# Kernel optimization log

Hardware: AMD Instinct MI355X
Metric: run time of the kernel (lower is better)

The kernel has to match this reference:

```python
import jax, jax.numpy as jnp
import numpy as np

WIDTH, DEPTH = 2048, 8
TIME_MOD = 30 * DEPTH + 2  # 242


def setup_inputs() -> dict:
    key = jax.random.key(0)
    ks = jax.random.split(key, 7)
    s = float(np.sqrt(1.0 / WIDTH))
    so = float(np.sqrt(1.0 / (WIDTH + DEPTH + 1)))
    return {
        "x": jax.random.normal(ks[0], (WIDTH,), dtype=jnp.float32),
        "weights": jax.random.uniform(ks[1], (WIDTH, WIDTH, DEPTH), minval=-s, maxval=s, dtype=jnp.float32),
        "output_weights": jax.random.uniform(ks[2], (WIDTH, DEPTH + 1), minval=-so, maxval=so, dtype=jnp.float32),
        "state": jax.random.uniform(ks[3], (WIDTH, DEPTH + 1), dtype=jnp.float32),  # relu outputs >= 0
        "stored_activations": jax.random.uniform(ks[4], (WIDTH, DEPTH + 1, TIME_MOD), dtype=jnp.float32),
        "stored_gradiets": jax.random.normal(ks[5], (WIDTH, DEPTH), dtype=jnp.float32),
        "output_gradient": jax.random.normal(ks[6], (WIDTH, DEPTH + 1, TIME_MOD), dtype=jnp.float32),
        "time": 7,
    }


def reference(x, weights, output_weights, state, stored_activations, stored_gradiets, output_gradient, time):
    width, dp1 = state.shape
    depth = dp1 - 1
    mod = 30 * depth + 2
    dt = state.dtype

    # recurrent state update: state[w,d] = relu(sum_i weights[i,w,d] * state_prev[i,d])
    hidden = jax.nn.relu(jnp.einsum("iwd,id->wd", weights, state[:, :depth]))
    state = jnp.concatenate([x[:, None], hidden], axis=1)  # (W, depth+1)
    output = jnp.sum(output_weights * state)

    # scatter into circular buffers at slot `time` (static int)
    sa = stored_activations.at[:, :, time].set(state)
    og = output_gradient.at[:, :, time].set(output_weights)

    # stored gradients: loop over a reads only OLD stored_gradiets[:, a+1] -> vectorizable
    a = np.arange(depth - 1)  # a = 0 .. depth-2 (static indices)
    t_idx = (time - 2 * depth + 2 * (a + 1)) % mod  # (depth-1,)
    relu_m = (sa[:, a + 2, (t_idx + 1) % mod] > 0).astype(dt)  # (W, depth-1)
    contrib = jnp.einsum("ija,ja->ia", weights[:, :, 1:depth], stored_gradiets[:, 1:depth])
    sg_head = relu_m * contrib + og[:, a + 1, t_idx]  # (W, depth-1)
    sg_last = og[:, depth, time]  # a == depth-1 branch (time_index == time)
    sg = jnp.concatenate([sg_head, sg_last[:, None]], axis=1)  # (W, depth)

    output_weights_gradient = state

    # weight eligibility traces (uses UPDATED sa and UPDATED sg)
    aa = np.arange(depth)
    tia = (time - 2 * depth + 2 * (aa + 1)) % mod  # (depth,)
    relu_g = (sa[:, aa + 1, tia] > 0).astype(dt)  # (W, depth)
    act_prev = sa[:, aa, (tia - 1) % mod]  # (W, depth)
    gradients = act_prev[:, None, :] * (sg * relu_g)[None, :, :]  # (W, W, depth)

    return output, state, sa, sg, og, gradients, output_weights_gradient
```

## Files before the change

### kernel.cpp

```cpp
#include <hip/hip_runtime.h>

#define MOD 242

static constexpr long long OFF_STATE = 1;
static constexpr long long OFF_SA    = 18433;
static constexpr long long OFF_SG    = 4478977;
static constexpr long long OFF_OG    = 4495361;
static constexpr long long OFF_GRAD  = 8955905;
static constexpr long long OFF_OWG   = 42510337;

#define WS_HID  0
#define WS_CON  524288
#define WS_COL  786432
#define WS_ROW  802816
#define WS_OUTP 819200

template <int CTRL, int RM>
__device__ __forceinline__ float dppadd(float x) {
  int t = __builtin_amdgcn_update_dpp(0, __float_as_int(x), CTRL, RM, 0xF, true);
  return x + __int_as_float(t);
}
__device__ __forceinline__ float wave_sum_dpp(float x) {
  x = dppadd<0x111, 0xF>(x);
  x = dppadd<0x112, 0xF>(x);
  x = dppadd<0x114, 0xF>(x);
  x = dppadd<0x118, 0xF>(x);
  x = dppadd<0x142, 0xA>(x);
  x = dppadd<0x143, 0xC>(x);
  return x;
}

__global__ __launch_bounds__(256) void k_mvcopy(
    const float* __restrict__ weights, const float* __restrict__ state,
    const float* __restrict__ sgrad, const float* __restrict__ sa_in,
    const float* __restrict__ og_in, float* __restrict__ ws,
    float* __restrict__ out)
{
  const int b   = blockIdx.x;
  const int tid = threadIdx.x;

  if (b >= 512) {
    const unsigned g = (unsigned)(b - 512) * 256u + (unsigned)tid;
    for (size_t e = g; e < 4460544u; e += 1114112u) {
      out[OFF_SA + e] = sa_in[e];
      out[OFF_OG + e] = og_in[e];
    }
    return;
  }

  const int iblk = b & 31;
  const int wblk = b >> 5;
  const int i0   = iblk * 64;
  const int w0   = wblk * 128;
  const int wv   = tid >> 6;
  const int l    = tid & 63;
  const int wgrp = wv >> 1;
  const int dh   = wv & 1;
  const int w    = w0 + wgrp * 64 + l;

  __shared__ __align__(16) float state_lds[64 * 8];
  __shared__ __align__(16) float cl[4][64][4];

  for (int idx = tid; idx < 64 * 8; idx += 256)
    state_lds[idx] = state[(size_t)(i0 + (idx >> 3)) * 9 + (idx & 7)];
  __syncthreads();

  const float4 sg4 = *(const float4*)&sgrad[(size_t)w * 8 + dh * 4];
  float4 h4 = make_float4(0.f, 0.f, 0.f, 0.f);
  const float* wp = weights + ((size_t)i0 * 2048 + w) * 8 + dh * 4;

  #pragma unroll 4
  for (int ii = 0; ii < 64; ++ii) {
    const float4 w4 = *(const float4*)wp;
    wp += 16384;
    const float4 s4 = *(const float4*)&state_lds[ii * 8 + dh * 4];

    h4.x = fmaf(w4.x, s4.x, h4.x);
    h4.y = fmaf(w4.y, s4.y, h4.y);
    h4.z = fmaf(w4.z, s4.z, h4.z);
    h4.w = fmaf(w4.w, s4.w, h4.w);

    float vx = wave_sum_dpp(w4.x * sg4.x);
    float vy = wave_sum_dpp(w4.y * sg4.y);
    float vz = wave_sum_dpp(w4.z * sg4.z);
    float vw = wave_sum_dpp(w4.w * sg4.w);
    if (l == 63)
      *(float4*)&cl[wv][ii][0] = make_float4(vx, vy, vz, vw);
  }

  *(float4*)&ws[WS_HID + ((size_t)iblk * 2048 + w) * 8 + dh * 4] = h4;

  __syncthreads();
  {
    const int ii = tid >> 2, q = tid & 3;
    const float c0 = cl[0][ii][q] + cl[2][ii][q];
    const float c1 = cl[1][ii][q] + cl[3][ii][q];
    const size_t base = WS_CON + ((size_t)wblk * 2048 + i0 + ii) * 8;
    ws[base + q]     = c0;
    ws[base + 4 + q] = c1;
  }
}

__global__ __launch_bounds__(64) void k_finalize(
    const float* __restrict__ x, const float* __restrict__ ow,
    const float* __restrict__ sa_in, const float* __restrict__ og_in,
    const int* __restrict__ timep, float* __restrict__ ws, float* __restrict__ out)
{
  const int r = blockIdx.x * 64 + threadIdx.x;
  const int t = *timep;

  float hid[8] = {0,0,0,0,0,0,0,0};
  {
    const float4* hp = (const float4*)&ws[WS_HID + (size_t)r * 8];
    #pragma unroll
    for (int ib = 0; ib < 32; ++ib) {
      const float4 pa = hp[(size_t)ib * 4096];
      const float4 pb = hp[(size_t)ib * 4096 + 1];
      hid[0] += pa.x; hid[1] += pa.y; hid[2] += pa.z; hid[3] += pa.w;
      hid[4] += pb.x; hid[5] += pb.y; hid[6] += pb.z; hid[7] += pb.w;
    }
  }
  float con[8] = {0,0,0,0,0,0,0,0};
  {
    const float4* cp = (const float4*)&ws[WS_CON + (size_t)r * 8];
    #pragma unroll
    for (int wb = 0; wb < 16; ++wb) {
      const float4 pa = cp[(size_t)wb * 4096];
      const float4 pb = cp[(size_t)wb * 4096 + 1];
      con[0] += pa.x; con[1] += pa.y; con[2] += pa.z; con[3] += pa.w;
      con[4] += pb.x; con[5] += pb.y; con[6] += pb.z; con[7] += pb.w;
    }
  }

  float s[9];
  s[0] = x[r];
  #pragma unroll
  for (int d = 0; d < 8; ++d) s[d + 1] = fmaxf(hid[d], 0.f);

  float owr[9];
  #pragma unroll
  for (int c = 0; c < 9; ++c) owr[c] = ow[(size_t)r * 9 + c];

  float p = 0.f;
  #pragma unroll
  for (int c = 0; c < 9; ++c) {
    out[OFF_STATE + (size_t)r * 9 + c] = s[c];
    out[OFF_OWG   + (size_t)r * 9 + c] = s[c];
    out[OFF_SA + ((size_t)r * 9 + c) * MOD + t] = s[c];
    out[OFF_OG + ((size_t)r * 9 + c) * MOD + t] = owr[c];
    p = fmaf(owr[c], s[c], p);
  }
  #pragma unroll
  for (int m = 1; m < 64; m <<= 1) p += __shfl_xor(p, m);
  if (threadIdx.x == 0) ws[WS_OUTP + blockIdx.x] = p;

  float sg[8];
  #pragma unroll
  for (int a = 0; a < 7; ++a) {
    const int ti = (t + 2 * a - 14 + MOD) % MOD;
    const int tm = (ti + 1) % MOD;
    const float av  = (tm == t) ? s[a + 2] : sa_in[((size_t)r * 9 + a + 2) * MOD + tm];
    const float ogv = (ti == t) ? owr[a + 1] : og_in[((size_t)r * 9 + a + 1) * MOD + ti];
    sg[a] = (av > 0.f ? con[a + 1] : 0.f) + ogv;
  }
  sg[7] = owr[8];
  #pragma unroll
  for (int a = 0; a < 8; ++a) out[OFF_SG + (size_t)r * 8 + a] = sg[a];

  #pragma unroll
  for (int aa = 0; aa < 8; ++aa) {
    const int ti = (t + 2 * aa - 14 + MOD) % MOD;
    const int tp = (ti - 1 + MOD) % MOD;
    const float rv = (ti == t) ? s[aa + 1] : sa_in[((size_t)r * 9 + aa + 1) * MOD + ti];
    const float ap = (tp == t) ? s[aa]     : sa_in[((size_t)r * 9 + aa) * MOD + tp];
    ws[WS_COL + r * 8 + aa] = (rv > 0.f) ? sg[aa] : 0.f;
    ws[WS_ROW + r * 8 + aa] = ap;
  }
}

__global__ __launch_bounds__(256) void k_grad(
    const float* __restrict__ ws, float* __restrict__ out)
{
  const int i = blockIdx.x;
  const int tid = threadIdx.x;
  if (i == 0 && tid == 0) {
    float s = 0.f;
    #pragma unroll
    for (int k = 0; k < 32; ++k) s += ws[WS_OUTP + k];
    out[0] = s;
  }
  const float rf = ws[WS_ROW + i * 8 + (tid & 7)];
  float* o = out + OFF_GRAD + (size_t)i * 16384;
  const float* cf = ws + WS_COL;
  #pragma unroll 4
  for (int k = 0; k < 64; ++k) {
    const int e = k * 256 + tid;
    o[e] = rf * cf[e];
  }
}

extern "C" void kernel_launch(void* const* d_in, const int* in_sizes, int n_in,
                              void* d_out, int out_size, void* d_ws, size_t ws_size,
                              hipStream_t stream)
{
  (void)in_sizes; (void)n_in; (void)out_size; (void)ws_size;
  const float* x     = (const float*)d_in[0];
  const float* wts   = (const float*)d_in[1];
  const float* ow    = (const float*)d_in[2];
  const float* st    = (const float*)d_in[3];
  const float* sa_in = (const float*)d_in[4];
  const float* sgrad = (const float*)d_in[5];
  const float* og_in = (const float*)d_in[6];
  const int*   timep = (const int*)d_in[7];
  float* out = (float*)d_out;
  float* ws  = (float*)d_ws;

  k_mvcopy<<<4864, 256, 0, stream>>>(wts, st, sgrad, sa_in, og_in, ws, out);
  k_finalize<<<32, 64, 0, stream>>>(x, ow, sa_in, og_in, timep, ws, out);
  k_grad<<<2048, 256, 0, stream>>>(ws, out);
}
```

Baseline: 336.0 us.

## Parallelize finalize kernel with one block per row and shuffle reductions

Restructures k_finalize from 32 blocks of 64 threads, one thread per row, to 2048 blocks of 256 threads, one block per row. The partial hidden and contribution sums are reduced with wave shuffles and LDS, and the per-row dot-product partials are written per row. k_grad's block 0 now reduces 2048 output partials instead of 32. The aim is to remove a latency-bound serial stage with very few threads, at the cost of more launch blocks, extra syncs and a bigger final reduction.

```diff
diff --git a/kernel.cpp b/kernel.cpp
--- a/kernel.cpp
+++ b/kernel.cpp
@@ -101,80 +101,83 @@
   }
 }
 
-__global__ __launch_bounds__(64) void k_finalize(
+__global__ __launch_bounds__(256) void k_finalize(
     const float* __restrict__ x, const float* __restrict__ ow,
     const float* __restrict__ sa_in, const float* __restrict__ og_in,
     const int* __restrict__ timep, float* __restrict__ ws, float* __restrict__ out)
 {
-  const int r = blockIdx.x * 64 + threadIdx.x;
-  const int t = *timep;
-
-  float hid[8] = {0,0,0,0,0,0,0,0};
+  const int r   = blockIdx.x;
+  const int tid = threadIdx.x;
+  const int wv  = tid >> 6;
+  const int l   = tid & 63;
+  const int t   = *timep;
+
+  __shared__ float hred[4][8];
+  __shared__ float cred[2][8];
+  __shared__ float s_sh[9];
+  __shared__ float owr_sh[9];
+
+  float hv = ws[WS_HID + ((size_t)(tid >> 3) * 2048 + r) * 8 + (tid & 7)];
+  hv += __shfl_xor(hv, 8);
+  hv += __shfl_xor(hv, 16);
+  hv += __shfl_xor(hv, 32);
+  if (l < 8) hred[wv][l] = hv;
+
+  float cv = 0.f;
+  if (tid < 128) cv = ws[WS_CON + ((size_t)(tid >> 3) * 2048 + r) * 8 + (tid & 7)];
+  cv += __shfl_xor(cv, 8);
+  cv += __shfl_xor(cv, 16);
+  cv += __shfl_xor(cv, 32);
+  if (wv < 2 && l < 8) cred[wv][l] = cv;
+
+  if (tid < 8 + 8)  {  }
+  if (tid >= 16 && tid < 25) owr_sh[tid - 16] = ow[(size_t)r * 9 + (tid - 16)];
+  if (tid == 8) s_sh[0] = x[r];
+  __syncthreads();
+
+  if (tid < 8) s_sh[tid + 1] = fmaxf(hred[0][tid] + hred[1][tid] + hred[2][tid] + hred[3][tid], 0.f);
+  __syncthreads();
+
+  if (tid < 9) {
+    const int c = tid;
+    const float sc = s_sh[c], owc = owr_sh[c];
+    out[OFF_STATE + (size_t)r * 9 + c] = sc;
+    out[OFF_OWG   + (size_t)r * 9 + c] = sc;
+    out[OFF_SA + ((size_t)r * 9 + c) * MOD + t] = sc;
+    out[OFF_OG + ((size_t)r * 9 + c) * MOD + t] = owc;
+  }
   {
-    const float4* hp = (const float4*)&ws[WS_HID + (size_t)r * 8];
-    #pragma unroll
-    for (int ib = 0; ib < 32; ++ib) {
-      const float4 pa = hp[(size_t)ib * 4096];
-      const float4 pb = hp[(size_t)ib * 4096 + 1];
-      hid[0] += pa.x; hid[1] += pa.y; hid[2] += pa.z; hid[3] += pa.w;
-      hid[4] += pb.x; hid[5] += pb.y; hid[6] += pb.z; hid[7] += pb.w;
+    float pterm = (tid < 9) ? s_sh[tid] * owr_sh[tid] : 0.f;
+    if (wv == 0) {
+      pterm += __shfl_xor(pterm, 1);
+      pterm += __shfl_xor(pterm, 2);
+      pterm += __shfl_xor(pterm, 4);
+      pterm += __shfl_xor(pterm, 8);
+      if (l == 0) ws[WS_OUTP + r] = pterm;
     }
   }
-  float con[8] = {0,0,0,0,0,0,0,0};
-  {
-    const float4* cp = (const float4*)&ws[WS_CON + (size_t)r * 8];
-    #pragma unroll
-    for (int wb = 0; wb < 16; ++wb) {
-      const float4 pa = cp[(size_t)wb * 4096];
-      const float4 pb = cp[(size_t)wb * 4096 + 1];
-      con[0] += pa.x; con[1] += pa.y; con[2] += pa.z; con[3] += pa.w;
-      con[4] += pb.x; con[5] += pb.y; con[6] += pb.z; con[7] += pb.w;
+
+  if (tid < 8) {
+    const int a = tid;
+    float sg;
+    if (a < 7) {
+      const int ti = (t + 2 * a - 14 + MOD) % MOD;
+      const int tm = (ti + 1) % MOD;
+      const float av  = (tm == t) ? s_sh[a + 2] : sa_in[((size_t)r * 9 + a + 2) * MOD + tm];
+      const float ogv = (ti == t) ? owr_sh[a + 1] : og_in[((size_t)r * 9 + a + 1) * MOD + ti];
+      const float con_a1 = cred[0][a + 1] + cred[1][a + 1];
+      sg = (av > 0.f ? con_a1 : 0.f) + ogv;
+    } else {
+      sg = owr_sh[8];
     }
-  }
-
-  float s[9];
-  s[0] = x[r];
-  #pragma unroll
-  for (int d = 0; d < 8; ++d) s[d + 1] = fmaxf(hid[d], 0.f);
-
-  float owr[9];
-  #pragma unroll
-  for (int c = 0; c < 9; ++c) owr[c] = ow[(size_t)r * 9 + c];
-
-  float p = 0.f;
-  #pragma unroll
-  for (int c = 0; c < 9; ++c) {
-    out[OFF_STATE + (size_t)r * 9 + c] = s[c];
-    out[OFF_OWG   + (size_t)r * 9 + c] = s[c];
-    out[OFF_SA + ((size_t)r * 9 + c) * MOD + t] = s[c];
-    out[OFF_OG + ((size_t)r * 9 + c) * MOD + t] = owr[c];
-    p = fmaf(owr[c], s[c], p);
-  }
-  #pragma unroll
-  for (int m = 1; m < 64; m <<= 1) p += __shfl_xor(p, m);
-  if (threadIdx.x == 0) ws[WS_OUTP + blockIdx.x] = p;
-
-  float sg[8];
-  #pragma unroll
-  for (int a = 0; a < 7; ++a) {
+    out[OFF_SG + (size_t)r * 8 + a] = sg;
+
     const int ti = (t + 2 * a - 14 + MOD) % MOD;
-    const int tm = (ti + 1) % MOD;
-    const float av  = (tm == t) ? s[a + 2] : sa_in[((size_t)r * 9 + a + 2) * MOD + tm];
-    const float ogv = (ti == t) ? owr[a + 1] : og_in[((size_t)r * 9 + a + 1) * MOD + ti];
-    sg[a] = (av > 0.f ? con[a + 1] : 0.f) + ogv;
-  }
-  sg[7] = owr[8];
-  #pragma unroll
-  for (int a = 0; a < 8; ++a) out[OFF_SG + (size_t)r * 8 + a] = sg[a];
-
-  #pragma unroll
-  for (int aa = 0; aa < 8; ++aa) {
-    const int ti = (t + 2 * aa - 14 + MOD) % MOD;
     const int tp = (ti - 1 + MOD) % MOD;
-    const float rv = (ti == t) ? s[aa + 1] : sa_in[((size_t)r * 9 + aa + 1) * MOD + ti];
-    const float ap = (tp == t) ? s[aa]     : sa_in[((size_t)r * 9 + aa) * MOD + tp];
-    ws[WS_COL + r * 8 + aa] = (rv > 0.f) ? sg[aa] : 0.f;
-    ws[WS_ROW + r * 8 + aa] = ap;
+    const float rv = (ti == t) ? s_sh[a + 1] : sa_in[((size_t)r * 9 + a + 1) * MOD + ti];
+    const float ap = (tp == t) ? s_sh[a]     : sa_in[((size_t)r * 9 + a) * MOD + tp];
+    ws[WS_COL + r * 8 + a] = (rv > 0.f) ? sg : 0.f;
+    ws[WS_ROW + r * 8 + a] = ap;
   }
 }
 
@@ -183,11 +186,16 @@
 {
   const int i = blockIdx.x;
   const int tid = threadIdx.x;
-  if (i == 0 && tid == 0) {
+  if (i == 0) {
     float s = 0.f;
     #pragma unroll
-    for (int k = 0; k < 32; ++k) s += ws[WS_OUTP + k];
-    out[0] = s;
+    for (int k = 0; k < 8; ++k) s += ws[WS_OUTP + k * 256 + tid];
+    #pragma unroll
+    for (int m = 1; m < 64; m <<= 1) s += __shfl_xor(s, m);
+    __shared__ float wsum[4];
+    if ((tid & 63) == 0) wsum[tid >> 6] = s;
+    __syncthreads();
+    if (tid == 0) out[0] = wsum[0] + wsum[1] + wsum[2] + wsum[3];
   }
   const float rf = ws[WS_ROW + i * 8 + (tid & 7)];
   float* o = out + OFF_GRAD + (size_t)i * 16384;
@@ -216,6 +224,6 @@
   float* ws  = (float*)d_ws;
 
   k_mvcopy<<<4864, 256, 0, stream>>>(wts, st, sgrad, sa_in, og_in, ws, out);
-  k_finalize<<<32, 64, 0, stream>>>(x, ow, sa_in, og_in, timep, ws, out);
+  k_finalize<<<2048, 256, 0, stream>>>(x, ow, sa_in, og_in, timep, ws, out);
   k_grad<<<2048, 256, 0, stream>>>(ws, out);
 }
```

New measurement: 334.8 us. Within noise of the previous version (-0.4%).
